# Optimization experiments

Measured on AMD Instinct MI355X. Metric: run time of the kernel, lower is better.

## Reference

```python
import jax, jax.numpy as jnp
import numpy as np

N_NODES = 100000
N_EDGES = 6400000
IN_CH = 128
HID = 32
OUT = 16


def setup_inputs() -> dict:
    key = jax.random.key(0)
    k1, k2, k3, k4 = jax.random.split(key, 4)
    x = jax.random.normal(k1, (N_NODES, IN_CH), dtype=jnp.float32)
    edge_index = jax.random.randint(k2, (2, N_EDGES), 0, N_NODES, dtype=jnp.int64)
    # Glorot-style init like PyG GCNConv
    W1 = jax.random.normal(k3, (IN_CH, HID), dtype=jnp.float32) * (1.0 / np.sqrt(IN_CH))
    b1 = jnp.zeros((HID,), dtype=jnp.float32)
    W2 = jax.random.normal(k4, (HID, OUT), dtype=jnp.float32) * (1.0 / np.sqrt(HID))
    b2 = jnp.zeros((OUT,), dtype=jnp.float32)
    return {"x": x, "edge_index": edge_index, "W1": W1, "b1": b1, "W2": W2, "b2": b2}


def _gcn_layer(h, W, b, row, col, norm, n_nodes):
    # transform then propagate (PyG GCNConv order)
    m = h @ W                                   # [N, F_out]
    msg = m[row] * norm[:, None]                # gather + scale, [E+N, F_out]
    agg = jax.ops.segment_sum(msg, col, num_segments=n_nodes)
    return agg + b


def reference(x, edge_index, W1, b1, W2, b2):
    n = x.shape[0]
    loops = jnp.arange(n, dtype=edge_index.dtype)
    row = jnp.concatenate([edge_index[0], loops])  # source
    col = jnp.concatenate([edge_index[1], loops])  # target (aggregation index)
    # symmetric GCN normalization with self-loops; deg >= 1 always
    deg = jax.ops.segment_sum(jnp.ones_like(col, dtype=x.dtype), col, num_segments=n)
    deg_inv_sqrt = jax.lax.rsqrt(deg)
    norm = deg_inv_sqrt[row] * deg_inv_sqrt[col]
    h = jax.nn.relu(_gcn_layer(x, W1, b1, row, col, norm, n))
    # dropout p=0.5 is identity in eval mode
    return _gcn_layer(h, W2, b2, row, col, norm, n)
```

## Files before the change

### kernel.cpp

```cpp
#include <hip/hip_runtime.h>
#include <hip/hip_bf16.h>

#define IN_CH 128
#define HID 32
#define OUT_CH 16
#define NPW 128
#define NPW_SHIFT 7
#define NB_MAX 1024
#define CAPF 12800
#define FBT 512
#define CAP 12288
#define SCAN_CHUNK 1024
#define NXCD 8
#define EPT 8

typedef int vint4 __attribute__((ext_vector_type(4)));
typedef vint4 vint4u __attribute__((aligned(4)));

__global__ void detect_dtype(const void* ei, long long ecount, int n, int* flag) {
    int lane = threadIdx.x;
    const long long* p = (const long long*)ei;
    long long st = ecount / 64; if (st < 1) st = 1;
    long long idx = (long long)lane * st;
    bool ok = true;
    if (idx < ecount) {
        long long v = p[idx];
        ok = (v >= 0 && v < n);
    }
    unsigned long long mask = __ballot(ok);
    if (lane == 0) *flag = (mask == ~0ULL) ? 1 : 0;
}

__device__ __forceinline__ int load_idx(const void* ei, long long i, int is64) {
    return is64 ? (int)((const long long*)ei)[i] : ((const int*)ei)[i];
}

__device__ __forceinline__ void load_idx8_nt(const void* ei, long long off, int is64,
                                             int* c) {
    if (is64) {
        const long long* p = (const long long*)ei + off;
#pragma unroll
        for (int j = 0; j < 8; ++j) c[j] = (int)__builtin_nontemporal_load(p + j);
    } else {
        vint4 v0 = __builtin_nontemporal_load((const vint4*)((const int*)ei + off));
        vint4 v1 = __builtin_nontemporal_load((const vint4*)((const int*)ei + off + 4));
        c[0] = v0.x; c[1] = v0.y; c[2] = v0.z; c[3] = v0.w;
        c[4] = v1.x; c[5] = v1.y; c[6] = v1.z; c[7] = v1.w;
    }
}

__device__ __forceinline__ float bf_lo(unsigned int u) { return __uint_as_float(u << 16); }
__device__ __forceinline__ float bf_hi(unsigned int u) { return __uint_as_float(u & 0xFFFF0000u); }

__global__ __launch_bounds__(256) void zero_int(int* p, int n) {
    int i = blockIdx.x * 256 + threadIdx.x;
    if (i < n) p[i] = 0;
}

__global__ __launch_bounds__(256) void zero_float(float* p, long long n) {
    long long i = (long long)blockIdx.x * 256 + threadIdx.x;
    if (i < n) p[i] = 0.f;
}

__global__ __launch_bounds__(FBT) void bucket_hist(const void* ei, long long E,
                                                   const int* flag, int* bhist,
                                                   int nb, long long chunk, int fbgrid) {
    __shared__ int hist[NB_MAX];
    for (int i = threadIdx.x; i < nb; i += FBT) hist[i] = 0;
    __syncthreads();
    long long lo = (long long)blockIdx.x * chunk;
    long long hi = lo + chunk; if (hi > E) hi = E;
    int is64 = *flag;
    if ((E & 7) == 0) {
        for (long long e = lo + (long long)threadIdx.x * EPT; e + EPT <= hi;
             e += (long long)FBT * EPT) {
            int c[8]; load_idx8_nt(ei, E + e, is64, c);
#pragma unroll
            for (int j = 0; j < 8; ++j) atomicAdd(&hist[c[j] >> NPW_SHIFT], 1);
        }
    } else {
        for (long long e = lo + threadIdx.x; e < hi; e += FBT)
            atomicAdd(&hist[load_idx(ei, E + e, is64) >> NPW_SHIFT], 1);
    }
    __syncthreads();
    for (int b = threadIdx.x; b < nb; b += FBT)
        bhist[(long long)b * fbgrid + blockIdx.x] = hist[b];
}

__global__ __launch_bounds__(256) void scan_blocks(int* bhist, int* btot, int nb,
                                                   int fbgrid) {
    __shared__ int sd[256];
    int b = blockIdx.x, t = threadIdx.x;
    int* p = bhist + (long long)b * fbgrid;
    int running = 0;
    for (int j0 = 0; j0 < fbgrid; j0 += 256) {
        int j = j0 + t;
        int v = (j < fbgrid) ? p[j] : 0;
        sd[t] = v; __syncthreads();
        for (int off = 1; off < 256; off <<= 1) {
            int u = (t >= off) ? sd[t - off] : 0;
            __syncthreads(); sd[t] += u; __syncthreads();
        }
        if (j < fbgrid) p[j] = running + sd[t] - v;
        int tot = sd[255];
        __syncthreads();
        running += tot;
    }
    if (t == 0) btot[b] = running;
}

__global__ __launch_bounds__(1024) void scan_buckets(const int* btot, int* bstart, int nb) {
    __shared__ int sd[1024];
    int t = threadIdx.x;
    int a0 = (2 * t < nb) ? btot[2 * t] : 0;
    int a1 = (2 * t + 1 < nb) ? btot[2 * t + 1] : 0;
    sd[t] = a0 + a1; __syncthreads();
    for (int off = 1; off < 1024; off <<= 1) {
        int v = (t >= off) ? sd[t - off] : 0;
        __syncthreads(); sd[t] += v; __syncthreads();
    }
    int excl = sd[t] - (a0 + a1);
    if (2 * t < nb)     bstart[2 * t] = excl;
    if (2 * t + 1 < nb) bstart[2 * t + 1] = excl + a0;
    if (t == 1023) bstart[nb] = sd[t];
}

__global__ __launch_bounds__(FBT) void fill_sort(const void* ei, long long E,
                                                 const int* flag, const int* bhist,
                                                 const int* bstart, int* bucketed,
                                                 int nb, long long chunk, int fbgrid) {
    __shared__ int lds[CAPF];
    __shared__ int hist[NB_MAX];
    __shared__ int base[NB_MAX];
    __shared__ int cur[NB_MAX];
    int blk = blockIdx.x, t = threadIdx.x;
    long long lo = (long long)blk * chunk;
    long long hi = lo + chunk; if (hi > E) hi = E;
    int cnt = (int)(hi - lo);
    for (int i = t; i < nb; i += FBT) hist[i] = 0;
    __syncthreads();
    int is64 = *flag;
    bool vec = ((E & 7) == 0) && ((chunk & 7) == 0);

    if (vec) {
        for (long long e = lo + (long long)t * EPT; e + EPT <= hi; e += (long long)FBT * EPT) {
            int c[8]; load_idx8_nt(ei, E + e, is64, c);
#pragma unroll
            for (int j = 0; j < 8; ++j) atomicAdd(&hist[c[j] >> NPW_SHIFT], 1);
        }
    } else {
        for (long long e = lo + t; e < hi; e += FBT)
            atomicAdd(&hist[load_idx(ei, E + e, is64) >> NPW_SHIFT], 1);
    }
    __syncthreads();

    if (cnt <= CAPF) {
        int a0 = (2 * t < nb) ? hist[2 * t] : 0;
        int a1 = (2 * t + 1 < nb) ? hist[2 * t + 1] : 0;
        base[t] = a0 + a1; __syncthreads();
        for (int off = 1; off < FBT; off <<= 1) {
            int u = (t >= off) ? base[t - off] : 0;
            __syncthreads(); base[t] += u; __syncthreads();
        }
        int incl = base[t];
        __syncthreads();
        int excl = incl - (a0 + a1);
        if (2 * t < nb)     { base[2 * t] = excl;          cur[2 * t] = excl; }
        if (2 * t + 1 < nb) { base[2 * t + 1] = excl + a0; cur[2 * t + 1] = excl + a0; }
        __syncthreads();

        if (vec) {
            for (long long e = lo + (long long)t * EPT; e + EPT <= hi; e += (long long)FBT * EPT) {
                int c[8], r[8];
                load_idx8_nt(ei, E + e, is64, c);
                load_idx8_nt(ei, e, is64, r);
#pragma unroll
                for (int j = 0; j < 8; ++j) {
                    int b = c[j] >> NPW_SHIFT;
                    int p = atomicAdd(&cur[b], 1);
                    lds[p] = r[j] | ((c[j] & (NPW - 1)) << 17);
                }
            }
        } else {
            for (long long e = lo + t; e < hi; e += FBT) {
                int col = load_idx(ei, E + e, is64);
                int row = load_idx(ei, e, is64);
                int b = col >> NPW_SHIFT;
                int p = atomicAdd(&cur[b], 1);
                lds[p] = row | ((col & (NPW - 1)) << 17);
            }
        }
        __syncthreads();

        int grp = t >> 4, lane = t & 15;
        for (int b = grp; b < nb; b += 32) {
            int l0 = base[b], c0 = hist[b];
            if (!c0) continue;
            int g0 = bstart[b] + bhist[(long long)b * fbgrid + blk];
            for (int j = lane; j < c0; j += 16)
                bucketed[g0 + j] = lds[l0 + j];
        }
    } else {
        for (int b = t; b < nb; b += FBT)
            cur[b] = bstart[b] + bhist[(long long)b * fbgrid + blk];
        __syncthreads();
        for (long long e = lo + t; e < hi; e += FBT) {
            int col = load_idx(ei, E + e, is64);
            int row = load_idx(ei, e, is64);
            int b = col >> NPW_SHIFT;
            int p = atomicAdd(&cur[b], 1);
            bucketed[p] = row | ((col & (NPW - 1)) << 17);
        }
    }
}

__global__ __launch_bounds__(512) void csr_sort(const int* __restrict__ bucketed,
                                                const int* __restrict__ bstart,
                                                int* __restrict__ csr,
                                                int* __restrict__ offs,
                                                float* __restrict__ dinv,
                                                int nb, int n) {
    __shared__ int lds_e[CAP];
    __shared__ int hist[NPW];
    __shared__ int cur[NPW];
    int b = blockIdx.x, t = threadIdx.x;
    int s0 = bstart[b], s1 = bstart[b + 1];
    int cnt = s1 - s0;
    if (t < NPW) hist[t] = 0;
    __syncthreads();
    bool fit = (cnt <= CAP);
    int cnt4 = cnt & ~3;
    if (fit) {
        for (int i = t * 4; i < cnt4; i += 2048) {
            vint4u e4 = *(const vint4u*)(bucketed + s0 + i);
            lds_e[i + 0] = e4.x; atomicAdd(&hist[e4.x >> 17], 1);
            lds_e[i + 1] = e4.y; atomicAdd(&hist[e4.y >> 17], 1);
            lds_e[i + 2] = e4.z; atomicAdd(&hist[e4.z >> 17], 1);
            lds_e[i + 3] = e4.w; atomicAdd(&hist[e4.w >> 17], 1);
        }
        for (int i = cnt4 + t; i < cnt; i += 512) {
            int e = bucketed[s0 + i];
            lds_e[i] = e;
            atomicAdd(&hist[e >> 17], 1);
        }
    } else {
        for (int i = t * 4; i < cnt4; i += 2048) {
            vint4u e4 = *(const vint4u*)(bucketed + s0 + i);
            atomicAdd(&hist[e4.x >> 17], 1);
            atomicAdd(&hist[e4.y >> 17], 1);
            atomicAdd(&hist[e4.z >> 17], 1);
            atomicAdd(&hist[e4.w >> 17], 1);
        }
        for (int i = cnt4 + t; i < cnt; i += 512)
            atomicAdd(&hist[bucketed[s0 + i] >> 17], 1);
    }
    __syncthreads();
    if (t == 0) {
        int run = 0;
        for (int k = 0; k < NPW; ++k) { cur[k] = run; run += hist[k]; }
    }
    __syncthreads();
    if (t < NPW) {
        int node = b * NPW + t;
        if (node < n) {
            offs[node] = s0 + cur[t];
            dinv[node] = 1.0f / sqrtf((float)(hist[t] + 1));
        }
    }
    if (b == nb - 1 && t == 0) offs[n] = s1;
    __syncthreads();
    if (fit) {
        for (int i = t; i < cnt; i += 512) {
            int e = lds_e[i];
            int pos = atomicAdd(&cur[e >> 17], 1);
            csr[s0 + pos] = e & 0x1FFFF;
        }
    } else {
        for (int i = t; i < cnt; i += 512) {
            int e = bucketed[s0 + i];
            int pos = atomicAdd(&cur[e >> 17], 1);
            csr[s0 + pos] = e & 0x1FFFF;
        }
    }
}

template <int BF16>
__global__ __launch_bounds__(256) void gemm1p(const float* __restrict__ x,
                                              const float* __restrict__ W1,
                                              const float* __restrict__ dinv,
                                              float* __restrict__ m1f,
                                              __hip_bfloat16* __restrict__ m1b, int n) {
    __shared__ float sW[IN_CH * HID];
    __shared__ float sx[8][IN_CH];
    for (int i = threadIdx.x; i < IN_CH * HID; i += 256) sW[i] = W1[i];
    int g = threadIdx.x >> 5;
    int c = threadIdx.x & 31;
    long long node = (long long)blockIdx.x * 8 + g;
    bool active = node < n;
    if (active) {
        const float4* xr = (const float4*)(x + node * IN_CH);
        float4 v = xr[c];
        sx[g][c * 4 + 0] = v.x; sx[g][c * 4 + 1] = v.y;
        sx[g][c * 4 + 2] = v.z; sx[g][c * 4 + 3] = v.w;
    }
    __syncthreads();
    if (!active) return;
    float acc = 0.f;
#pragma unroll
    for (int k = 0; k < IN_CH; ++k)
        acc = fmaf(sx[g][k], sW[k * HID + c], acc);
    float v = acc * dinv[node];
    if (BF16) m1b[(node << 5) + c] = __float2bfloat16(v);
    else      m1f[(node << 5) + c] = v;
}

template <int BF16>
__global__ __launch_bounds__(256) void gemm2p(const float* __restrict__ h,
                                              const float* __restrict__ W2,
                                              const float* __restrict__ dinv,
                                              float* __restrict__ m2f,
                                              __hip_bfloat16* __restrict__ m2b, int n) {
    __shared__ float sW[HID * OUT_CH];
    for (int i = threadIdx.x; i < HID * OUT_CH; i += 256) sW[i] = W2[i];
    __syncthreads();
    long long t = (long long)blockIdx.x * 256 + threadIdx.x;
    long long node = t >> 4;
    int c = (int)(t & 15);
    if (node >= n) return;
    const float* hr = h + node * HID;
    float acc = 0.f;
#pragma unroll
    for (int k = 0; k < HID; ++k)
        acc = fmaf(hr[k], sW[k * OUT_CH + c], acc);
    float v = acc * dinv[node];
    if (BF16) m2b[(node << 4) + c] = __float2bfloat16(v);
    else      m2f[(node << 4) + c] = v;
}

__global__ __launch_bounds__(256) void agg1_bf(const unsigned int* __restrict__ m1b,
                                               const int* __restrict__ csr,
                                               const int* __restrict__ offs,
                                               const float* __restrict__ dinv,
                                               const float* __restrict__ b1,
                                               float* __restrict__ h, int n) {
    int g = threadIdx.x >> 4;
    int c = threadIdx.x & 15;
    long long node = (long long)blockIdx.x * 16 + g;
    if (node >= n) return;
    unsigned int us = m1b[(node << 4) + c];
    float accL = bf_lo(us), accH = bf_hi(us);
    int s = offs[node], e1 = offs[node + 1];
    for (; s + 7 < e1; s += 8) {
        vint4u a = *(const vint4u*)(csr + s);
        vint4u b = *(const vint4u*)(csr + s + 4);
        unsigned int u0 = m1b[((long long)a.x << 4) + c];
        unsigned int u1 = m1b[((long long)a.y << 4) + c];
        unsigned int u2 = m1b[((long long)a.z << 4) + c];
        unsigned int u3 = m1b[((long long)a.w << 4) + c];
        unsigned int u4 = m1b[((long long)b.x << 4) + c];
        unsigned int u5 = m1b[((long long)b.y << 4) + c];
        unsigned int u6 = m1b[((long long)b.z << 4) + c];
        unsigned int u7 = m1b[((long long)b.w << 4) + c];
        accL += bf_lo(u0); accH += bf_hi(u0);
        accL += bf_lo(u1); accH += bf_hi(u1);
        accL += bf_lo(u2); accH += bf_hi(u2);
        accL += bf_lo(u3); accH += bf_hi(u3);
        accL += bf_lo(u4); accH += bf_hi(u4);
        accL += bf_lo(u5); accH += bf_hi(u5);
        accL += bf_lo(u6); accH += bf_hi(u6);
        accL += bf_lo(u7); accH += bf_hi(u7);
    }
    for (; s < e1; ++s) {
        unsigned int u = m1b[((long long)csr[s] << 4) + c];
        accL += bf_lo(u); accH += bf_hi(u);
    }
    float di = dinv[node];
    float vL = accL * di + b1[2 * c];
    float vH = accH * di + b1[2 * c + 1];
    float2 val;
    val.x = vL > 0.f ? vL : 0.f;
    val.y = vH > 0.f ? vH : 0.f;
    *(float2*)(h + (node << 5) + 2 * c) = val;
}

__global__ __launch_bounds__(256) void agg2_bf(const unsigned int* __restrict__ m2b,
                                               const int* __restrict__ csr,
                                               const int* __restrict__ offs,
                                               const float* __restrict__ dinv,
                                               const float* __restrict__ b2,
                                               float* __restrict__ out, int n) {
    int g = threadIdx.x >> 3;
    int c = threadIdx.x & 7;
    long long node = (long long)blockIdx.x * 32 + g;
    if (node >= n) return;
    unsigned int us = m2b[(node << 3) + c];
    float accL = bf_lo(us), accH = bf_hi(us);
    int s = offs[node], e1 = offs[node + 1];
    for (; s + 7 < e1; s += 8) {
        vint4u a = *(const vint4u*)(csr + s);
        vint4u b = *(const vint4u*)(csr + s + 4);
        unsigned int u0 = m2b[((long long)a.x << 3) + c];
        unsigned int u1 = m2b[((long long)a.y << 3) + c];
        unsigned int u2 = m2b[((long long)a.z << 3) + c];
        unsigned int u3 = m2b[((long long)a.w << 3) + c];
        unsigned int u4 = m2b[((long long)b.x << 3) + c];
        unsigned int u5 = m2b[((long long)b.y << 3) + c];
        unsigned int u6 = m2b[((long long)b.z << 3) + c];
        unsigned int u7 = m2b[((long long)b.w << 3) + c];
        accL += bf_lo(u0); accH += bf_hi(u0);
        accL += bf_lo(u1); accH += bf_hi(u1);
        accL += bf_lo(u2); accH += bf_hi(u2);
        accL += bf_lo(u3); accH += bf_hi(u3);
        accL += bf_lo(u4); accH += bf_hi(u4);
        accL += bf_lo(u5); accH += bf_hi(u5);
        accL += bf_lo(u6); accH += bf_hi(u6);
        accL += bf_lo(u7); accH += bf_hi(u7);
    }
    for (; s < e1; ++s) {
        unsigned int u = m2b[((long long)csr[s] << 3) + c];
        accL += bf_lo(u); accH += bf_hi(u);
    }
    float di = dinv[node];
    float2 val;
    val.x = accL * di + b2[2 * c];
    val.y = accH * di + b2[2 * c + 1];
    *(float2*)(out + (node << 4) + 2 * c) = val;
}

__global__ __launch_bounds__(256) void count_edges(const void* ei, int* cnt,
                                                   long long E, const int* flag) {
    long long e0 = ((long long)blockIdx.x * 256 + threadIdx.x) * EPT;
    if (e0 >= E) return;
    int is64 = *flag;
    if (e0 + EPT <= E && (E & 7) == 0) {
        int c[EPT];
        load_idx8_nt(ei, E + e0, is64, c);
#pragma unroll
        for (int j = 0; j < EPT; ++j) atomicAdd(&cnt[c[j]], 1);
    } else {
        for (long long e = e0; e < E && e < e0 + EPT; ++e)
            atomicAdd(&cnt[load_idx(ei, E + e, is64)], 1);
    }
}

__global__ __launch_bounds__(256) void compute_dinv(const int* cnt, float* dinv, int n) {
    int i = blockIdx.x * 256 + threadIdx.x;
    if (i < n) dinv[i] = 1.0f / sqrtf((float)(cnt[i] + 1));
}

__global__ __launch_bounds__(256) void scan_partial(const int* cnt, int* partial, int n) {
    __shared__ int sd[256];
    int base = blockIdx.x * SCAN_CHUNK;
    int s = 0;
    for (int j = threadIdx.x; j < SCAN_CHUNK; j += 256) {
        int i = base + j;
        if (i < n) s += cnt[i];
    }
    sd[threadIdx.x] = s;
    __syncthreads();
    for (int off = 128; off > 0; off >>= 1) {
        if (threadIdx.x < off) sd[threadIdx.x] += sd[threadIdx.x + off];
        __syncthreads();
    }
    if (threadIdx.x == 0) partial[blockIdx.x] = sd[0];
}

__global__ void scan_serial(int* partial, int* offs, int nblk, int n) {
    if (threadIdx.x == 0 && blockIdx.x == 0) {
        int run = 0;
        for (int b = 0; b < nblk; ++b) { int t = partial[b]; partial[b] = run; run += t; }
        offs[n] = run;
    }
}

__global__ __launch_bounds__(256) void scan_final(const int* cnt, const int* partial,
                                                  int* offs, int n) {
    __shared__ int sd[256];
    int base = blockIdx.x * SCAN_CHUNK;
    int t = threadIdx.x;
    int loc[4]; int ts = 0;
#pragma unroll
    for (int j = 0; j < 4; ++j) {
        int i = base + t * 4 + j;
        loc[j] = (i < n) ? cnt[i] : 0;
        ts += loc[j];
    }
    sd[t] = ts;
    __syncthreads();
    for (int off = 1; off < 256; off <<= 1) {
        int v = (t >= off) ? sd[t - off] : 0;
        __syncthreads();
        sd[t] += v;
        __syncthreads();
    }
    int excl = sd[t] - ts + partial[blockIdx.x];
#pragma unroll
    for (int j = 0; j < 4; ++j) {
        int i = base + t * 4 + j;
        if (i < n) offs[i] = excl;
        excl += loc[j];
    }
}

__global__ __launch_bounds__(256) void copy_int(const int* src, int* dst, int n) {
    int i = blockIdx.x * 256 + threadIdx.x;
    if (i < n) dst[i] = src[i];
}

__global__ __launch_bounds__(256) void fill_csr_win(const void* ei, int* cursor, int* csr,
                                                    long long E, const int* flag,
                                                    int npw, int n) {
    int w = blockIdx.x & (NXCD - 1);
    int b = blockIdx.x >> 3;
    int lo = w * npw;
    int hi = lo + npw; if (hi > n) hi = n;
    long long e0 = ((long long)b * 256 + threadIdx.x) * EPT;
    if (e0 >= E) return;
    int is64 = *flag;
    if (e0 + EPT <= E && (E & 7) == 0) {
        int c[EPT];
        load_idx8_nt(ei, E + e0, is64, c);
#pragma unroll
        for (int j = 0; j < EPT; ++j) {
            if (c[j] >= lo && c[j] < hi) {
                int row = load_idx(ei, e0 + j, is64);
                int pos = atomicAdd(&cursor[c[j]], 1);
                csr[pos] = row;
            }
        }
    } else {
        for (long long e = e0; e < E && e < e0 + EPT; ++e) {
            int col = load_idx(ei, E + e, is64);
            if (col >= lo && col < hi) {
                int row = load_idx(ei, e, is64);
                int pos = atomicAdd(&cursor[col], 1);
                csr[pos] = row;
            }
        }
    }
}

__global__ __launch_bounds__(256) void scatter1(const float* __restrict__ m1s,
                                                const void* ei,
                                                float* __restrict__ h,
                                                long long E, const int* flag) {
    long long e = (long long)blockIdx.x * 8 + (threadIdx.x >> 5);
    int c = threadIdx.x & 31;
    if (e >= E) return;
    int is64 = *flag;
    int row = load_idx(ei, e, is64);
    int col = load_idx(ei, E + e, is64);
    atomicAdd(&h[(long long)col * HID + c], m1s[(long long)row * HID + c]);
}

__global__ __launch_bounds__(256) void fixup1(const float* __restrict__ m1s,
                                              const float* __restrict__ dinv,
                                              const float* __restrict__ b1,
                                              float* __restrict__ h, int n) {
    long long t = (long long)blockIdx.x * 256 + threadIdx.x;
    long long node = t >> 5; int c = (int)(t & 31);
    if (node >= n) return;
    float v = (h[node * HID + c] + m1s[node * HID + c]) * dinv[node] + b1[c];
    h[node * HID + c] = v > 0.f ? v : 0.f;
}

__global__ __launch_bounds__(256) void scatter2(const float* __restrict__ m2s,
                                                const void* ei,
                                                float* __restrict__ out,
                                                long long E, const int* flag) {
    long long e = (long long)blockIdx.x * 16 + (threadIdx.x >> 4);
    int c = threadIdx.x & 15;
    if (e >= E) return;
    int is64 = *flag;
    int row = load_idx(ei, e, is64);
    int col = load_idx(ei, E + e, is64);
    atomicAdd(&out[(long long)col * OUT_CH + c], m2s[(long long)row * OUT_CH + c]);
}

__global__ __launch_bounds__(256) void fixup2(const float* __restrict__ m2s,
                                              const float* __restrict__ dinv,
                                              const float* __restrict__ b2,
                                              float* __restrict__ out, int n) {
    long long t = (long long)blockIdx.x * 256 + threadIdx.x;
    long long node = t >> 4; int c = (int)(t & 15);
    if (node >= n) return;
    out[node * OUT_CH + c] = (out[node * OUT_CH + c] + m2s[node * OUT_CH + c]) * dinv[node] + b2[c];
}

extern "C" void kernel_launch(void* const* d_in, const int* in_sizes, int n_in,
                              void* d_out, int out_size, void* d_ws, size_t ws_size,
                              hipStream_t stream) {
    const float* x  = (const float*)d_in[0];
    const void*  ei = d_in[1];
    const float* W1 = (const float*)d_in[2];
    const float* b1 = (const float*)d_in[3];
    const float* W2 = (const float*)d_in[4];
    const float* b2 = (const float*)d_in[5];
    float* out = (float*)d_out;

    const int n = in_sizes[0] / IN_CH;
    const long long E = in_sizes[1] / 2;
    const int nb = (n + NPW - 1) / NPW;

    const long long chunkF = (((E + 511) / 512) + 7) & ~7LL;
    const int fbgrid = (int)((E + chunkF - 1) / chunkF);

    char* w = (char*)d_ws;
    size_t used = 0;
    auto carve = [&](size_t bytes) -> void* {
        void* p = (void*)(w + used);
        used += (bytes + 255) & ~(size_t)255;
        return p;
    };
    auto A = [](size_t b) -> size_t { return (b + 255) & ~(size_t)255; };

    int*   bstart  = (int*)carve((size_t)(NB_MAX + 1) * 4);
    int*   btot    = (int*)carve((size_t)NB_MAX * 4);
    float* dinv    = (float*)carve((size_t)n * 4);
    int*   flag    = (int*)carve(256);
    int*   offs    = (int*)carve((size_t)(n + 1) * 4);
    int*   cnt     = (int*)carve((size_t)n * 4);
    int*   partial = (int*)carve(4096);
    const size_t base = used;

    const size_t bhistB = A((size_t)nb * fbgrid * 4);
    const size_t mbB    = A((size_t)n * HID * 2);
    const size_t hB     = A((size_t)n * HID * 4);
    const size_t needT1 = base + bhistB + 2 * A((size_t)E * 4) + mbB + hB;
    const size_t needT2 = base + A((size_t)E * 4) + mbB + hB;
    const size_t needT3 = base + 2 * A((size_t)n * HID * 4);
    const bool tier1 = (ws_size >= needT1) && (n <= 131071) && (nb <= NB_MAX) &&
                       (chunkF <= CAPF || true);
    const bool tier2 = !tier1 && (ws_size >= needT2) && (n <= 131071);

    const int nblkN  = (n + 255) / 256;
    const int nblkEv = (int)((E + 256LL * EPT - 1) / (256LL * EPT));
    const int nblkSc = (n + SCAN_CHUNK - 1) / SCAN_CHUNK;
    const int nblkH  = (int)(((long long)n * HID + 255) / 256);
    const int nblkO  = (int)(((long long)n * OUT_CH + 255) / 256);

    detect_dtype<<<1, 64, 0, stream>>>(ei, E, n, flag);

    if (tier1) {
        int*   bhist    = (int*)carve((size_t)nb * fbgrid * 4);
        int*   bucketed = (int*)carve((size_t)E * 4);
        int*   csr      = (int*)carve((size_t)E * 4);
        __hip_bfloat16* m1b = (__hip_bfloat16*)carve((size_t)n * HID * 2);
        float* h  = (float*)carve((size_t)n * HID * 4);
        __hip_bfloat16* m2b = m1b;

        bucket_hist<<<fbgrid, FBT, 0, stream>>>(ei, E, flag, bhist, nb, chunkF, fbgrid);
        scan_blocks<<<nb, 256, 0, stream>>>(bhist, btot, nb, fbgrid);
        scan_buckets<<<1, 1024, 0, stream>>>(btot, bstart, nb);
        fill_sort<<<fbgrid, FBT, 0, stream>>>(ei, E, flag, bhist, bstart,
                                              bucketed, nb, chunkF, fbgrid);
        csr_sort<<<nb, 512, 0, stream>>>(bucketed, bstart, csr, offs, dinv, nb, n);

        gemm1p<1><<<(n + 7) / 8, 256, 0, stream>>>(x, W1, dinv, nullptr, m1b, n);
        agg1_bf<<<(n + 15) / 16, 256, 0, stream>>>((const unsigned int*)m1b, csr, offs,
                                                   dinv, b1, h, n);
        gemm2p<1><<<nblkO, 256, 0, stream>>>(h, W2, dinv, nullptr, m2b, n);
        agg2_bf<<<(n + 31) / 32, 256, 0, stream>>>((const unsigned int*)m2b, csr, offs,
                                                   dinv, b2, out, n);
    } else if (tier2) {
        int*   csr = (int*)carve((size_t)E * 4);
        __hip_bfloat16* m1b = (__hip_bfloat16*)carve((size_t)n * HID * 2);
        float* h  = (float*)carve((size_t)n * HID * 4);
        __hip_bfloat16* m2b = m1b;

        zero_int<<<nblkN, 256, 0, stream>>>(cnt, n);
        count_edges<<<nblkEv, 256, 0, stream>>>(ei, cnt, E, flag);
        compute_dinv<<<nblkN, 256, 0, stream>>>(cnt, dinv, n);
        scan_partial<<<nblkSc, 256, 0, stream>>>(cnt, partial, n);
        scan_serial<<<1, 64, 0, stream>>>(partial, offs, nblkSc, n);
        scan_final<<<nblkSc, 256, 0, stream>>>(cnt, partial, offs, n);
        copy_int<<<nblkN, 256, 0, stream>>>(offs, cnt, n);

        const int npw2 = (n + NXCD - 1) / NXCD;
        fill_csr_win<<<nblkEv * NXCD, 256, 0, stream>>>(ei, cnt, csr, E, flag, npw2, n);

        gemm1p<1><<<(n + 7) / 8, 256, 0, stream>>>(x, W1, dinv, nullptr, m1b, n);
        agg1_bf<<<(n + 15) / 16, 256, 0, stream>>>((const unsigned int*)m1b, csr, offs,
                                                   dinv, b1, h, n);
        gemm2p<1><<<nblkO, 256, 0, stream>>>(h, W2, dinv, nullptr, m2b, n);
        agg2_bf<<<(n + 31) / 32, 256, 0, stream>>>((const unsigned int*)m2b, csr, offs,
                                                   dinv, b2, out, n);
    } else if (ws_size >= needT3) {
        float* m1 = (float*)carve((size_t)n * HID * 4);
        float* h  = (float*)carve((size_t)n * HID * 4);
        float* m2 = m1;

        zero_int<<<nblkN, 256, 0, stream>>>(cnt, n);
        count_edges<<<nblkEv, 256, 0, stream>>>(ei, cnt, E, flag);
        compute_dinv<<<nblkN, 256, 0, stream>>>(cnt, dinv, n);

        gemm1p<0><<<(n + 7) / 8, 256, 0, stream>>>(x, W1, dinv, m1, nullptr, n);
        zero_float<<<nblkH, 256, 0, stream>>>(h, (long long)n * HID);
        scatter1<<<(int)((E + 7) / 8), 256, 0, stream>>>(m1, ei, h, E, flag);
        fixup1<<<nblkH, 256, 0, stream>>>(m1, dinv, b1, h, n);
        gemm2p<0><<<nblkO, 256, 0, stream>>>(h, W2, dinv, m2, nullptr, n);
        zero_float<<<nblkO, 256, 0, stream>>>(out, (long long)n * OUT_CH);
        scatter2<<<(int)((E + 15) / 16), 256, 0, stream>>>(m2, ei, out, E, flag);
        fixup2<<<nblkO, 256, 0, stream>>>(m2, dinv, b2, out, n);
    }
}
```

Measured before the change: 263.8 us.

## Split layer-1 aggregation by source half and reuse bucket histogram in fill_sort

csr_sort now sorts each node's edges by destination and by whether the source lies in the lower or upper half of nodes, and records a mid offset per node. Layer-1 aggregation runs as two passes, each gathering only from one half of m1b, so each pass touches a smaller working set that may stay in cache. The first pass stores partial sums with nontemporal writes and the second adds them back. Separately, fill_sort reads its per-block histogram from bucket_hist's output instead of recounting, which needs a second bexcl buffer. The cost is an extra kernel launch, an extra round trip of h through memory, and twice as many histogram keys in csr_sort.

New measurement: 270.1 us. +2.4%, slower.

```diff
diff --git a/kernel.cpp b/kernel.cpp
--- a/kernel.cpp
+++ b/kernel.cpp
@@ -10,12 +10,14 @@
 #define CAPF 12800
 #define FBT 512
 #define CAP 12288
+#define KEYS (NPW * 2)
 #define SCAN_CHUNK 1024
 #define NXCD 8
 #define EPT 8
 
 typedef int vint4 __attribute__((ext_vector_type(4)));
 typedef vint4 vint4u __attribute__((aligned(4)));
+typedef float vfloat2 __attribute__((ext_vector_type(2)));
 
 __global__ void detect_dtype(const void* ei, long long ecount, int n, int* flag) {
     int lane = threadIdx.x;
@@ -87,11 +89,12 @@
         bhist[(long long)b * fbgrid + blockIdx.x] = hist[b];
 }
 
-__global__ __launch_bounds__(256) void scan_blocks(int* bhist, int* btot, int nb,
-                                                   int fbgrid) {
+__global__ __launch_bounds__(256) void scan_blocks(const int* bhist, int* bexcl,
+                                                   int* btot, int nb, int fbgrid) {
     __shared__ int sd[256];
     int b = blockIdx.x, t = threadIdx.x;
-    int* p = bhist + (long long)b * fbgrid;
+    const int* p = bhist + (long long)b * fbgrid;
+    int* q = bexcl + (long long)b * fbgrid;
     int running = 0;
     for (int j0 = 0; j0 < fbgrid; j0 += 256) {
         int j = j0 + t;
@@ -101,7 +104,7 @@
             int u = (t >= off) ? sd[t - off] : 0;
             __syncthreads(); sd[t] += u; __syncthreads();
         }
-        if (j < fbgrid) p[j] = running + sd[t] - v;
+        if (j < fbgrid) q[j] = running + sd[t] - v;
         int tot = sd[255];
         __syncthreads();
         running += tot;
@@ -127,8 +130,9 @@
 
 __global__ __launch_bounds__(FBT) void fill_sort(const void* ei, long long E,
                                                  const int* flag, const int* bhist,
-                                                 const int* bstart, int* bucketed,
-                                                 int nb, long long chunk, int fbgrid) {
+                                                 const int* bexcl, const int* bstart,
+                                                 int* bucketed, int nb,
+                                                 long long chunk, int fbgrid) {
     __shared__ int lds[CAPF];
     __shared__ int hist[NB_MAX];
     __shared__ int base[NB_MAX];
@@ -137,22 +141,11 @@
     long long lo = (long long)blk * chunk;
     long long hi = lo + chunk; if (hi > E) hi = E;
     int cnt = (int)(hi - lo);
-    for (int i = t; i < nb; i += FBT) hist[i] = 0;
+    for (int b = t; b < nb; b += FBT)
+        hist[b] = bhist[(long long)b * fbgrid + blk];
     __syncthreads();
     int is64 = *flag;
     bool vec = ((E & 7) == 0) && ((chunk & 7) == 0);
-
-    if (vec) {
-        for (long long e = lo + (long long)t * EPT; e + EPT <= hi; e += (long long)FBT * EPT) {
-            int c[8]; load_idx8_nt(ei, E + e, is64, c);
-#pragma unroll
-            for (int j = 0; j < 8; ++j) atomicAdd(&hist[c[j] >> NPW_SHIFT], 1);
-        }
-    } else {
-        for (long long e = lo + t; e < hi; e += FBT)
-            atomicAdd(&hist[load_idx(ei, E + e, is64) >> NPW_SHIFT], 1);
-    }
-    __syncthreads();
 
     if (cnt <= CAPF) {
         int a0 = (2 * t < nb) ? hist[2 * t] : 0;
@@ -196,13 +189,13 @@
         for (int b = grp; b < nb; b += 32) {
             int l0 = base[b], c0 = hist[b];
             if (!c0) continue;
-            int g0 = bstart[b] + bhist[(long long)b * fbgrid + blk];
+            int g0 = bstart[b] + bexcl[(long long)b * fbgrid + blk];
             for (int j = lane; j < c0; j += 16)
                 bucketed[g0 + j] = lds[l0 + j];
         }
     } else {
         for (int b = t; b < nb; b += FBT)
-            cur[b] = bstart[b] + bhist[(long long)b * fbgrid + blk];
+            cur[b] = bstart[b] + bexcl[(long long)b * fbgrid + blk];
         __syncthreads();
         for (long long e = lo + t; e < hi; e += FBT) {
             int col = load_idx(ei, E + e, is64);
@@ -218,53 +211,58 @@
                                                 const int* __restrict__ bstart,
                                                 int* __restrict__ csr,
                                                 int* __restrict__ offs,
+                                                int* __restrict__ mid,
                                                 float* __restrict__ dinv,
-                                                int nb, int n) {
+                                                int nb, int n, int nhalf) {
     __shared__ int lds_e[CAP];
-    __shared__ int hist[NPW];
-    __shared__ int cur[NPW];
+    __shared__ int histk[KEYS];
+    __shared__ int cur[KEYS];
     int b = blockIdx.x, t = threadIdx.x;
     int s0 = bstart[b], s1 = bstart[b + 1];
     int cnt = s1 - s0;
-    if (t < NPW) hist[t] = 0;
+    if (t < KEYS) histk[t] = 0;
     __syncthreads();
     bool fit = (cnt <= CAP);
     int cnt4 = cnt & ~3;
+    auto key = [&](int e) {
+        return (((e >> 17) & (NPW - 1)) << 1) | (((e & 0x1FFFF) >= nhalf) ? 1 : 0);
+    };
     if (fit) {
         for (int i = t * 4; i < cnt4; i += 2048) {
             vint4u e4 = *(const vint4u*)(bucketed + s0 + i);
-            lds_e[i + 0] = e4.x; atomicAdd(&hist[e4.x >> 17], 1);
-            lds_e[i + 1] = e4.y; atomicAdd(&hist[e4.y >> 17], 1);
-            lds_e[i + 2] = e4.z; atomicAdd(&hist[e4.z >> 17], 1);
-            lds_e[i + 3] = e4.w; atomicAdd(&hist[e4.w >> 17], 1);
+            lds_e[i + 0] = e4.x; atomicAdd(&histk[key(e4.x)], 1);
+            lds_e[i + 1] = e4.y; atomicAdd(&histk[key(e4.y)], 1);
+            lds_e[i + 2] = e4.z; atomicAdd(&histk[key(e4.z)], 1);
+            lds_e[i + 3] = e4.w; atomicAdd(&histk[key(e4.w)], 1);
         }
         for (int i = cnt4 + t; i < cnt; i += 512) {
             int e = bucketed[s0 + i];
             lds_e[i] = e;
-            atomicAdd(&hist[e >> 17], 1);
+            atomicAdd(&histk[key(e)], 1);
         }
     } else {
         for (int i = t * 4; i < cnt4; i += 2048) {
             vint4u e4 = *(const vint4u*)(bucketed + s0 + i);
-            atomicAdd(&hist[e4.x >> 17], 1);
-            atomicAdd(&hist[e4.y >> 17], 1);
-            atomicAdd(&hist[e4.z >> 17], 1);
-            atomicAdd(&hist[e4.w >> 17], 1);
+            atomicAdd(&histk[key(e4.x)], 1);
+            atomicAdd(&histk[key(e4.y)], 1);
+            atomicAdd(&histk[key(e4.z)], 1);
+            atomicAdd(&histk[key(e4.w)], 1);
         }
         for (int i = cnt4 + t; i < cnt; i += 512)
-            atomicAdd(&hist[bucketed[s0 + i] >> 17], 1);
+            atomicAdd(&histk[key(bucketed[s0 + i])], 1);
     }
     __syncthreads();
     if (t == 0) {
         int run = 0;
-        for (int k = 0; k < NPW; ++k) { cur[k] = run; run += hist[k]; }
+        for (int k = 0; k < KEYS; ++k) { cur[k] = run; run += histk[k]; }
     }
     __syncthreads();
     if (t < NPW) {
         int node = b * NPW + t;
         if (node < n) {
-            offs[node] = s0 + cur[t];
-            dinv[node] = 1.0f / sqrtf((float)(hist[t] + 1));
+            offs[node] = s0 + cur[2 * t];
+            mid[node]  = s0 + cur[2 * t] + histk[2 * t];
+            dinv[node] = 1.0f / sqrtf((float)(histk[2 * t] + histk[2 * t + 1] + 1));
         }
     }
     if (b == nb - 1 && t == 0) offs[n] = s1;
@@ -272,13 +270,13 @@
     if (fit) {
         for (int i = t; i < cnt; i += 512) {
             int e = lds_e[i];
-            int pos = atomicAdd(&cur[e >> 17], 1);
+            int pos = atomicAdd(&cur[key(e)], 1);
             csr[s0 + pos] = e & 0x1FFFF;
         }
     } else {
         for (int i = t; i < cnt; i += 512) {
             int e = bucketed[s0 + i];
-            int pos = atomicAdd(&cur[e >> 17], 1);
+            int pos = atomicAdd(&cur[key(e)], 1);
             csr[s0 + pos] = e & 0x1FFFF;
         }
     }
@@ -337,9 +335,11 @@
     else      m2f[(node << 4) + c] = v;
 }
 
+template <int MODE>
 __global__ __launch_bounds__(256) void agg1_bf(const unsigned int* __restrict__ m1b,
                                                const int* __restrict__ csr,
                                                const int* __restrict__ offs,
+                                               const int* __restrict__ mid,
                                                const float* __restrict__ dinv,
                                                const float* __restrict__ b1,
                                                float* __restrict__ h, int n) {
@@ -347,9 +347,16 @@
     int c = threadIdx.x & 15;
     long long node = (long long)blockIdx.x * 16 + g;
     if (node >= n) return;
-    unsigned int us = m1b[(node << 4) + c];
-    float accL = bf_lo(us), accH = bf_hi(us);
-    int s = offs[node], e1 = offs[node + 1];
+    int s, e1;
+    if (MODE == 0)      { s = offs[node]; e1 = mid[node]; }
+    else if (MODE == 1) { s = mid[node];  e1 = offs[node + 1]; }
+    else                { s = offs[node]; e1 = offs[node + 1]; }
+    float accL, accH;
+    if (MODE == 0) { accL = 0.f; accH = 0.f; }
+    else {
+        unsigned int us = m1b[(node << 4) + c];
+        accL = bf_lo(us); accH = bf_hi(us);
+    }
     for (; s + 7 < e1; s += 8) {
         vint4u a = *(const vint4u*)(csr + s);
         vint4u b = *(const vint4u*)(csr + s + 4);
@@ -374,13 +381,22 @@
         unsigned int u = m1b[((long long)csr[s] << 4) + c];
         accL += bf_lo(u); accH += bf_hi(u);
     }
-    float di = dinv[node];
-    float vL = accL * di + b1[2 * c];
-    float vH = accH * di + b1[2 * c + 1];
-    float2 val;
-    val.x = vL > 0.f ? vL : 0.f;
-    val.y = vH > 0.f ? vH : 0.f;
-    *(float2*)(h + (node << 5) + 2 * c) = val;
+    if (MODE == 0) {
+        vfloat2 val; val.x = accL; val.y = accH;
+        __builtin_nontemporal_store(val, (vfloat2*)(h + (node << 5) + 2 * c));
+    } else {
+        if (MODE == 1) {
+            vfloat2 prev = __builtin_nontemporal_load((const vfloat2*)(h + (node << 5) + 2 * c));
+            accL += prev.x; accH += prev.y;
+        }
+        float di = dinv[node];
+        float vL = accL * di + b1[2 * c];
+        float vH = accH * di + b1[2 * c + 1];
+        vfloat2 val;
+        val.x = vL > 0.f ? vL : 0.f;
+        val.y = vH > 0.f ? vH : 0.f;
+        *(vfloat2*)(h + (node << 5) + 2 * c) = val;
+    }
 }
 
 __global__ __launch_bounds__(256) void agg2_bf(const unsigned int* __restrict__ m2b,
@@ -421,10 +437,10 @@
         accL += bf_lo(u); accH += bf_hi(u);
     }
     float di = dinv[node];
-    float2 val;
+    vfloat2 val;
     val.x = accL * di + b2[2 * c];
     val.y = accH * di + b2[2 * c + 1];
-    *(float2*)(out + (node << 4) + 2 * c) = val;
+    *(vfloat2*)(out + (node << 4) + 2 * c) = val;
 }
 
 __global__ __launch_bounds__(256) void count_edges(const void* ei, int* cnt,
@@ -601,6 +617,7 @@
     const int n = in_sizes[0] / IN_CH;
     const long long E = in_sizes[1] / 2;
     const int nb = (n + NPW - 1) / NPW;
+    const int nhalf = (n + 1) / 2;
 
     const long long chunkF = (((E + 511) / 512) + 7) & ~7LL;
     const int fbgrid = (int)((E + chunkF - 1) / chunkF);
@@ -619,6 +636,7 @@
     float* dinv    = (float*)carve((size_t)n * 4);
     int*   flag    = (int*)carve(256);
     int*   offs    = (int*)carve((size_t)(n + 1) * 4);
+    int*   mid     = (int*)carve((size_t)n * 4);
     int*   cnt     = (int*)carve((size_t)n * 4);
     int*   partial = (int*)carve(4096);
     const size_t base = used;
@@ -626,11 +644,10 @@
     const size_t bhistB = A((size_t)nb * fbgrid * 4);
     const size_t mbB    = A((size_t)n * HID * 2);
     const size_t hB     = A((size_t)n * HID * 4);
-    const size_t needT1 = base + bhistB + 2 * A((size_t)E * 4) + mbB + hB;
+    const size_t needT1 = base + 2 * bhistB + 2 * A((size_t)E * 4) + mbB + hB;
     const size_t needT2 = base + A((size_t)E * 4) + mbB + hB;
     const size_t needT3 = base + 2 * A((size_t)n * HID * 4);
-    const bool tier1 = (ws_size >= needT1) && (n <= 131071) && (nb <= NB_MAX) &&
-                       (chunkF <= CAPF || true);
+    const bool tier1 = (ws_size >= needT1) && (n <= 131071) && (nb <= NB_MAX);
     const bool tier2 = !tier1 && (ws_size >= needT2) && (n <= 131071);
 
     const int nblkN  = (n + 255) / 256;
@@ -643,6 +660,7 @@
 
     if (tier1) {
         int*   bhist    = (int*)carve((size_t)nb * fbgrid * 4);
+        int*   bexcl    = (int*)carve((size_t)nb * fbgrid * 4);
         int*   bucketed = (int*)carve((size_t)E * 4);
         int*   csr      = (int*)carve((size_t)E * 4);
         __hip_bfloat16* m1b = (__hip_bfloat16*)carve((size_t)n * HID * 2);
@@ -650,15 +668,18 @@
         __hip_bfloat16* m2b = m1b;
 
         bucket_hist<<<fbgrid, FBT, 0, stream>>>(ei, E, flag, bhist, nb, chunkF, fbgrid);
-        scan_blocks<<<nb, 256, 0, stream>>>(bhist, btot, nb, fbgrid);
+        scan_blocks<<<nb, 256, 0, stream>>>(bhist, bexcl, btot, nb, fbgrid);
         scan_buckets<<<1, 1024, 0, stream>>>(btot, bstart, nb);
-        fill_sort<<<fbgrid, FBT, 0, stream>>>(ei, E, flag, bhist, bstart,
+        fill_sort<<<fbgrid, FBT, 0, stream>>>(ei, E, flag, bhist, bexcl, bstart,
                                               bucketed, nb, chunkF, fbgrid);
-        csr_sort<<<nb, 512, 0, stream>>>(bucketed, bstart, csr, offs, dinv, nb, n);
+        csr_sort<<<nb, 512, 0, stream>>>(bucketed, bstart, csr, offs, mid, dinv,
+                                         nb, n, nhalf);
 
         gemm1p<1><<<(n + 7) / 8, 256, 0, stream>>>(x, W1, dinv, nullptr, m1b, n);
-        agg1_bf<<<(n + 15) / 16, 256, 0, stream>>>((const unsigned int*)m1b, csr, offs,
-                                                   dinv, b1, h, n);
+        agg1_bf<0><<<(n + 15) / 16, 256, 0, stream>>>((const unsigned int*)m1b, csr,
+                                                      offs, mid, dinv, b1, h, n);
+        agg1_bf<1><<<(n + 15) / 16, 256, 0, stream>>>((const unsigned int*)m1b, csr,
+                                                      offs, mid, dinv, b1, h, n);
         gemm2p<1><<<nblkO, 256, 0, stream>>>(h, W2, dinv, nullptr, m2b, n);
         agg2_bf<<<(n + 31) / 32, 256, 0, stream>>>((const unsigned int*)m2b, csr, offs,
                                                    dinv, b2, out, n);
@@ -680,8 +701,8 @@
         fill_csr_win<<<nblkEv * NXCD, 256, 0, stream>>>(ei, cnt, csr, E, flag, npw2, n);
 
         gemm1p<1><<<(n + 7) / 8, 256, 0, stream>>>(x, W1, dinv, nullptr, m1b, n);
-        agg1_bf<<<(n + 15) / 16, 256, 0, stream>>>((const unsigned int*)m1b, csr, offs,
-                                                   dinv, b1, h, n);
+        agg1_bf<2><<<(n + 15) / 16, 256, 0, stream>>>((const unsigned int*)m1b, csr,
+                                                      offs, offs, dinv, b1, h, n);
         gemm2p<1><<<nblkO, 256, 0, stream>>>(h, W2, dinv, nullptr, m2b, n);
         agg2_bf<<<(n + 31) / 32, 256, 0, stream>>>((const unsigned int*)m2b, csr, offs,
                                                    dinv, b2, out, n);
```
